# Performance work log

Hardware: AMD Instinct MI355X
Metric: run time of the kernel (lower is better)

## Reference

```python
import jax, jax.numpy as jnp
import numpy as np

B = 2048          # batch
F = 32            # input feature size
H = 512           # lstm hidden size
BN = 64           # autoencoder bottleneck
OUT = 8           # final dense output size
SEQ_LEN = 128
LOOK_AHEAD = 32
RS, RE = 0, 8     # replace_start, replace_end (RE-RS == OUT)


def setup_inputs() -> dict:
    key = jax.random.key(0)
    ks = jax.random.split(key, 16)
    s = lambda k, shape: (jax.random.normal(k, shape, jnp.float32) * 0.05)
    return {
        'x': jax.random.normal(ks[0], (B, SEQ_LEN + LOOK_AHEAD, F), jnp.float32),
        # layer-0 LSTMCell (input F)
        'Wih0': s(ks[1], (F, 4 * H)), 'Whh0': s(ks[2], (H, 4 * H)),
        'bih0': s(ks[3], (4 * H,)),   'bhh0': s(ks[4], (4 * H,)),
        # layer-1 LSTMCell (input H)
        'Wih1': s(ks[5], (H, 4 * H)), 'Whh1': s(ks[6], (H, 4 * H)),
        'bih1': s(ks[7], (4 * H,)),   'bhh1': s(ks[8], (4 * H,)),
        # discretizing autoencoder: 2H -> BN -> 2H (shared across layers)
        'We': s(ks[9], (2 * H, BN)),  'be': s(ks[10], (BN,)),
        'Wd': s(ks[11], (BN, 2 * H)), 'bd': s(ks[12], (2 * H,)),
        # final dense H -> OUT
        'Wf': s(ks[13], (H, OUT)),    'bf': s(ks[14], (OUT,)),
    }


def _lstm_cell(x, h, c, Wih, Whh, bih, bhh):
    # torch.nn.LSTMCell gate order: i, f, g, o
    g = x @ Wih + bih + h @ Whh + bhh          # [B, 4H]
    i, f, gg, o = jnp.split(g, 4, axis=1)
    i, f, o = jax.nn.sigmoid(i), jax.nn.sigmoid(f), jax.nn.sigmoid(o)
    c2 = f * c + i * jnp.tanh(gg)
    return o * jnp.tanh(c2), c2


def _ae(z, We, be, Wd, bd):
    # bottleneck with straight-through rounding (discretization)
    b = jnp.tanh(z @ We + be)
    q = b + jax.lax.stop_gradient(jnp.round(b) - b)
    return q @ Wd + bd


def _layers_fwd(x_t, st, p):
    h0, c0, h1, c1 = st
    hc = _ae(jnp.concatenate([h0, c0], axis=1), p['We'], p['be'], p['Wd'], p['bd'])
    h0, c0 = jnp.split(hc, 2, axis=1)
    h0, c0 = _lstm_cell(x_t, h0, c0, p['Wih0'], p['Whh0'], p['bih0'], p['bhh0'])
    # dropout layer between stacked layers is identity in eval mode
    hc = _ae(jnp.concatenate([h1, c1], axis=1), p['We'], p['be'], p['Wd'], p['bd'])
    h1, c1 = jnp.split(hc, 2, axis=1)
    h1, c1 = _lstm_cell(h0, h1, c1, p['Wih1'], p['Whh1'], p['bih1'], p['bhh1'])
    return (h0, c0, h1, c1)


def reference(x, Wih0, Whh0, bih0, bhh0, Wih1, Whh1, bih1, bhh1,
              We, be, Wd, bd, Wf, bf):
    p = dict(Wih0=Wih0, Whh0=Whh0, bih0=bih0, bhh0=bhh0,
             Wih1=Wih1, Whh1=Whh1, bih1=bih1, bhh1=bhh1,
             We=We, be=be, Wd=Wd, bd=bd)
    bsz = x.shape[0]
    z = jnp.zeros((bsz, H), x.dtype)
    st = (z, z, z, z)

    # warm-up phase over seq_len observed steps
    def step1(st, x_t):
        return _layers_fwd(x_t, st, p), None
    st, _ = jax.lax.scan(step1, st, jnp.swapaxes(x[:, :SEQ_LEN], 0, 1))
    out0 = st[2] @ Wf + bf  # final dense on top-layer h

    def step2(carry, x_t):
        st, out = carry
        x_t = x_t.at[:, RS:RE].set(out)
        st = _layers_fwd(x_t, st, p)
        out = st[2] @ Wf + bf
        return (st, out), out
    (_, _), outs = jax.lax.scan(step2, (st, out0),
                                jnp.swapaxes(x[:, SEQ_LEN:SEQ_LEN + LOOK_AHEAD], 0, 1))

    # [B, 1 + look_ahead, OUT]
    return jnp.concatenate([out0[:, None, :], jnp.swapaxes(outs, 0, 1)], axis=1)
```

## Files before the change

### kernel.cpp

```cpp
#include <hip/hip_runtime.h>
#include <hip/hip_bf16.h>
#include <math.h>

#define NB    2048
#define FIN   32
#define HH    512
#define G4    2048
#define BNE   64
#define OUTD  8
#define SEQL  128
#define LOOK  32
#define TOT   (SEQL + LOOK)
#define TB    8
#define NTHR  1024

__device__ __forceinline__ float sigf(float v) { return 1.0f / (1.0f + expf(-v)); }

#define MAC2(S, HS)                                    \
  {                                                    \
    a[S].x = fmaf(w.x, (HS), a[S].x);                  \
    a[S].y = fmaf(w.y, (HS), a[S].y);                  \
  }
#define MAC2x8()                                       \
  {                                                    \
    MAC2(0, hA.x); MAC2(1, hA.y); MAC2(2, hA.z); MAC2(3, hA.w); \
    MAC2(4, hB.x); MAC2(5, hB.y); MAC2(6, hB.z); MAC2(7, hB.w); \
  }

__global__ __launch_bounds__(NTHR)
void fused_rnn(const float* __restrict__ x,
               const float* __restrict__ Wih0, const float* __restrict__ Whh0,
               const float* __restrict__ bih0, const float* __restrict__ bhh0,
               const float* __restrict__ Wih1, const float* __restrict__ Whh1,
               const float* __restrict__ bih1, const float* __restrict__ bhh1,
               const float* __restrict__ We,   const float* __restrict__ be,
               const float* __restrict__ Wd,   const float* __restrict__ bd,
               const float* __restrict__ Wf,   const float* __restrict__ bf,
               float* __restrict__ out)
{
  __shared__ float sh0[HH][TB], sc0[HH][TB], sh1[HH][TB], sc1[HH][TB];
  __shared__ float sg[TB][G4];
  __shared__ float sq[2][BNE][TB];
  __shared__ float sx[FIN][TB];
  __shared__ float sout[TB][OUTD];

  const int t  = threadIdx.x;
  const int b0 = blockIdx.x * TB;

  for (int i = t; i < HH * TB; i += NTHR) {
    (&sh0[0][0])[i] = 0.f; (&sc0[0][0])[i] = 0.f;
    (&sh1[0][0])[i] = 0.f; (&sc1[0][0])[i] = 0.f;
  }

  const float2 bb0 = make_float2(bih0[2*t]   + bhh0[2*t],
                                 bih0[2*t+1] + bhh0[2*t+1]);
  const float2 bb1 = make_float2(bih1[2*t]   + bhh1[2*t],
                                 bih1[2*t+1] + bhh1[2*t+1]);

  const double Athr = 0.5493061443340549;

  for (int step = 0; step < TOT; ++step) {
    __syncthreads();

    {
      const int ae = t >> 9, s = (t >> 6) & 7, n = t & 63;
      const float* Sh = ae ? &sh1[0][0] : &sh0[0][0];
      const float* Sc = ae ? &sc1[0][0] : &sc0[0][0];
      double a0 = (double)be[n];
      const float* we0 = We + n;
#pragma unroll 4
      for (int k = 0; k < HH; k++)
        a0 = fma((double)Sh[k * TB + s], (double)we0[(size_t)k * BNE], a0);
      const float* we1 = We + (size_t)HH * BNE + n;
#pragma unroll 4
      for (int k = 0; k < HH; k++)
        a0 = fma((double)Sc[k * TB + s], (double)we1[(size_t)k * BNE], a0);
      sq[ae][n][s] = (a0 > Athr) ? 1.f : ((a0 < -Athr) ? -1.f : 0.f);
    }
    __syncthreads();

    {
      float aq0[TB], aq1[TB];
      const float bdv = bd[t];
#pragma unroll
      for (int s = 0; s < TB; s++) { aq0[s] = bdv; aq1[s] = bdv; }
      const float* wd = Wd + t;
#pragma unroll 2
      for (int j = 0; j < BNE; j++) {
        const float w = wd[(size_t)j * (2 * HH)];
        const float4 qA0 = *(const float4*)&sq[0][j][0];
        const float4 qB0 = *(const float4*)&sq[0][j][4];
        const float4 qA1 = *(const float4*)&sq[1][j][0];
        const float4 qB1 = *(const float4*)&sq[1][j][4];
        aq0[0] = fmaf(qA0.x, w, aq0[0]); aq0[1] = fmaf(qA0.y, w, aq0[1]);
        aq0[2] = fmaf(qA0.z, w, aq0[2]); aq0[3] = fmaf(qA0.w, w, aq0[3]);
        aq0[4] = fmaf(qB0.x, w, aq0[4]); aq0[5] = fmaf(qB0.y, w, aq0[5]);
        aq0[6] = fmaf(qB0.z, w, aq0[6]); aq0[7] = fmaf(qB0.w, w, aq0[7]);
        aq1[0] = fmaf(qA1.x, w, aq1[0]); aq1[1] = fmaf(qA1.y, w, aq1[1]);
        aq1[2] = fmaf(qA1.z, w, aq1[2]); aq1[3] = fmaf(qA1.w, w, aq1[3]);
        aq1[4] = fmaf(qB1.x, w, aq1[4]); aq1[5] = fmaf(qB1.y, w, aq1[5]);
        aq1[6] = fmaf(qB1.z, w, aq1[6]); aq1[7] = fmaf(qB1.w, w, aq1[7]);
      }
      if (t < HH) {
#pragma unroll
        for (int s = 0; s < TB; s++) { sh0[t][s] = aq0[s]; sh1[t][s] = aq1[s]; }
      } else {
        const int c = t - HH;
#pragma unroll
        for (int s = 0; s < TB; s++) { sc0[c][s] = aq0[s]; sc1[c][s] = aq1[s]; }
      }
      if (t < FIN * TB) {
        int s = t >> 5, f = t & 31;
        float xv;
        if (step >= SEQL && f < OUTD) xv = sout[s][f];
        else xv = x[((size_t)(b0 + s) * TOT + step) * FIN + f];
        sx[f][s] = xv;
      }
    }
    __syncthreads();

    {
      float2 a[TB];
#pragma unroll
      for (int s = 0; s < TB; s++) a[s] = bb0;
      const float2* wx = (const float2*)Wih0 + t;
#pragma unroll 4
      for (int k = 0; k < FIN; k++) {
        const float2 w  = wx[(size_t)k * (G4 / 2)];
        const float4 hA = *(const float4*)&sx[k][0];
        const float4 hB = *(const float4*)&sx[k][4];
        MAC2x8();
      }
      const float2* wh = (const float2*)Whh0 + t;
#pragma unroll 8
      for (int k = 0; k < HH; k++) {
        const float2 w  = wh[(size_t)k * (G4 / 2)];
        const float4 hA = *(const float4*)&sh0[k][0];
        const float4 hB = *(const float4*)&sh0[k][4];
        MAC2x8();
      }
#pragma unroll
      for (int s = 0; s < TB; s++) *(float2*)&sg[s][2 * t] = a[s];
    }
    __syncthreads();
    {
      const int h  = t & (HH - 1);
      const int sb = (t >> 9) * 4;
#pragma unroll
      for (int s2 = 0; s2 < 4; s2++) {
        const int s = sb + s2;
        const float ig = sigf(sg[s][h]);
        const float fg = sigf(sg[s][HH + h]);
        const float gt = tanhf(sg[s][2 * HH + h]);
        const float og = sigf(sg[s][3 * HH + h]);
        const float c2 = fmaf(fg, sc0[h][s], ig * gt);
        sc0[h][s] = c2;
        sh0[h][s] = og * tanhf(c2);
      }
    }
    __syncthreads();

    {
      float2 a[TB];
#pragma unroll
      for (int s = 0; s < TB; s++) a[s] = bb1;
      const float2* wx = (const float2*)Wih1 + t;
#pragma unroll 8
      for (int k = 0; k < HH; k++) {
        const float2 w  = wx[(size_t)k * (G4 / 2)];
        const float4 hA = *(const float4*)&sh0[k][0];
        const float4 hB = *(const float4*)&sh0[k][4];
        MAC2x8();
      }
      const float2* wh = (const float2*)Whh1 + t;
#pragma unroll 8
      for (int k = 0; k < HH; k++) {
        const float2 w  = wh[(size_t)k * (G4 / 2)];
        const float4 hA = *(const float4*)&sh1[k][0];
        const float4 hB = *(const float4*)&sh1[k][4];
        MAC2x8();
      }
#pragma unroll
      for (int s = 0; s < TB; s++) *(float2*)&sg[s][2 * t] = a[s];
    }
    __syncthreads();
    {
      const int h  = t & (HH - 1);
      const int sb = (t >> 9) * 4;
#pragma unroll
      for (int s2 = 0; s2 < 4; s2++) {
        const int s = sb + s2;
        const float ig = sigf(sg[s][h]);
        const float fg = sigf(sg[s][HH + h]);
        const float gt = tanhf(sg[s][2 * HH + h]);
        const float og = sigf(sg[s][3 * HH + h]);
        const float c2 = fmaf(fg, sc1[h][s], ig * gt);
        sc1[h][s] = c2;
        sh1[h][s] = og * tanhf(c2);
      }
    }

    if (step >= SEQL - 1) {
      __syncthreads();
      if (t < TB * OUTD) {
        int s = t >> 3, o = t & 7;
        float a = bf[o];
#pragma unroll 4
        for (int k = 0; k < HH; k++) a = fmaf(sh1[k][s], Wf[k * OUTD + o], a);
        sout[s][o] = a;
        int slot = step - (SEQL - 1);
        out[((size_t)(b0 + s) * (1 + LOOK) + slot) * OUTD + o] = a;
      }
    }
  }
}

extern "C" void kernel_launch(void* const* d_in, const int* in_sizes, int n_in,
                              void* d_out, int out_size, void* d_ws, size_t ws_size,
                              hipStream_t stream) {
  const float* x    = (const float*)d_in[0];
  const float* Wih0 = (const float*)d_in[1];
  const float* Whh0 = (const float*)d_in[2];
  const float* bih0 = (const float*)d_in[3];
  const float* bhh0 = (const float*)d_in[4];
  const float* Wih1 = (const float*)d_in[5];
  const float* Whh1 = (const float*)d_in[6];
  const float* bih1 = (const float*)d_in[7];
  const float* bhh1 = (const float*)d_in[8];
  const float* We   = (const float*)d_in[9];
  const float* be   = (const float*)d_in[10];
  const float* Wd   = (const float*)d_in[11];
  const float* bd   = (const float*)d_in[12];
  const float* Wf   = (const float*)d_in[13];
  const float* bf   = (const float*)d_in[14];

  fused_rnn<<<NB / TB, NTHR, 0, stream>>>(x, Wih0, Whh0, bih0, bhh0,
                                          Wih1, Whh1, bih1, bhh1,
                                          We, be, Wd, bd, Wf, bf,
                                          (float*)d_out);
}
```

Baseline: 81.12 ms.

## Fuse LSTM gate activation into gate GEMV by remapping threads to hidden units

```diff
diff --git a/kernel.cpp b/kernel.cpp
--- a/kernel.cpp
+++ b/kernel.cpp
@@ -1,5 +1,4 @@
 #include <hip/hip_runtime.h>
-#include <hip/hip_bf16.h>
 #include <math.h>
 
 #define NB    2048
@@ -16,18 +15,11 @@
 
 __device__ __forceinline__ float sigf(float v) { return 1.0f / (1.0f + expf(-v)); }
 
-#define MAC2(S, HS)                                    \
-  {                                                    \
-    a[S].x = fmaf(w.x, (HS), a[S].x);                  \
-    a[S].y = fmaf(w.y, (HS), a[S].y);                  \
-  }
-#define MAC2x8()                                       \
-  {                                                    \
-    MAC2(0, hA.x); MAC2(1, hA.y); MAC2(2, hA.z); MAC2(3, hA.w); \
-    MAC2(4, hB.x); MAC2(5, hB.y); MAC2(6, hB.z); MAC2(7, hB.w); \
-  }
-
-__global__ __launch_bounds__(NTHR)
+#define GMAC2(A, W, HV)                                                  \
+  { A[0].x = fmaf((W).x, (HV).x, A[0].x); A[0].y = fmaf((W).y, (HV).x, A[0].y); \
+    A[1].x = fmaf((W).x, (HV).y, A[1].x); A[1].y = fmaf((W).y, (HV).y, A[1].y); }
+
+__global__ __launch_bounds__(NTHR, 4)
 void fused_rnn(const float* __restrict__ x,
                const float* __restrict__ Wih0, const float* __restrict__ Whh0,
                const float* __restrict__ bih0, const float* __restrict__ bhh0,
@@ -39,8 +31,7 @@
                float* __restrict__ out)
 {
   __shared__ float sh0[HH][TB], sc0[HH][TB], sh1[HH][TB], sc1[HH][TB];
-  __shared__ float sg[TB][G4];
-  __shared__ float sq[2][BNE][TB];
+  __shared__ float tq[2][BNE][TB];
   __shared__ float sx[FIN][TB];
   __shared__ float sout[TB][OUTD];
 
@@ -52,10 +43,21 @@
     (&sh1[0][0])[i] = 0.f; (&sc1[0][0])[i] = 0.f;
   }
 
-  const float2 bb0 = make_float2(bih0[2*t]   + bhh0[2*t],
-                                 bih0[2*t+1] + bhh0[2*t+1]);
-  const float2 bb1 = make_float2(bih1[2*t]   + bhh1[2*t],
-                                 bih1[2*t+1] + bhh1[2*t+1]);
+  const int q   = t & 255;
+  const int sh2 = t >> 8;
+  const int s2  = 2 * sh2;
+  const int u0  = 2 * q;
+  float2 bg0[4], bg1[4];
+#pragma unroll
+  for (int m = 0; m < 4; m++) {
+    const int c = m * HH + u0;
+    bg0[m] = make_float2(bih0[c] + bhh0[c], bih0[c + 1] + bhh0[c + 1]);
+    bg1[m] = make_float2(bih1[c] + bhh1[c], bih1[c + 1] + bhh1[c + 1]);
+  }
+
+  const int ae = t >> 9, sE = (t >> 6) & 7, n = t & 63;
+
+  const float bdc = bd[t];
 
   const double Athr = 0.5493061443340549;
 
@@ -63,51 +65,70 @@
     __syncthreads();
 
     {
-      const int ae = t >> 9, s = (t >> 6) & 7, n = t & 63;
       const float* Sh = ae ? &sh1[0][0] : &sh0[0][0];
       const float* Sc = ae ? &sc1[0][0] : &sc0[0][0];
       double a0 = (double)be[n];
-      const float* we0 = We + n;
+      const float* weh = We + n;
 #pragma unroll 4
       for (int k = 0; k < HH; k++)
-        a0 = fma((double)Sh[k * TB + s], (double)we0[(size_t)k * BNE], a0);
-      const float* we1 = We + (size_t)HH * BNE + n;
+        a0 = fma((double)Sh[k * TB + sE], (double)weh[(size_t)k * BNE], a0);
+      const float* wec = We + (size_t)HH * BNE + n;
 #pragma unroll 4
       for (int k = 0; k < HH; k++)
-        a0 = fma((double)Sc[k * TB + s], (double)we1[(size_t)k * BNE], a0);
-      sq[ae][n][s] = (a0 > Athr) ? 1.f : ((a0 < -Athr) ? -1.f : 0.f);
+        a0 = fma((double)Sc[k * TB + sE], (double)wec[(size_t)k * BNE], a0);
+      tq[ae][n][sE] = (a0 > Athr) ? 1.f : ((a0 < -Athr) ? -1.f : 0.f);
     }
     __syncthreads();
 
     {
-      float aq0[TB], aq1[TB];
-      const float bdv = bd[t];
+      float d0[TB], d1[TB];
 #pragma unroll
-      for (int s = 0; s < TB; s++) { aq0[s] = bdv; aq1[s] = bdv; }
+      for (int s = 0; s < TB; s++) { d0[s] = bdc; d1[s] = bdc; }
       const float* wd = Wd + t;
-#pragma unroll 2
-      for (int j = 0; j < BNE; j++) {
-        const float w = wd[(size_t)j * (2 * HH)];
-        const float4 qA0 = *(const float4*)&sq[0][j][0];
-        const float4 qB0 = *(const float4*)&sq[0][j][4];
-        const float4 qA1 = *(const float4*)&sq[1][j][0];
-        const float4 qB1 = *(const float4*)&sq[1][j][4];
-        aq0[0] = fmaf(qA0.x, w, aq0[0]); aq0[1] = fmaf(qA0.y, w, aq0[1]);
-        aq0[2] = fmaf(qA0.z, w, aq0[2]); aq0[3] = fmaf(qA0.w, w, aq0[3]);
-        aq0[4] = fmaf(qB0.x, w, aq0[4]); aq0[5] = fmaf(qB0.y, w, aq0[5]);
-        aq0[6] = fmaf(qB0.z, w, aq0[6]); aq0[7] = fmaf(qB0.w, w, aq0[7]);
-        aq1[0] = fmaf(qA1.x, w, aq1[0]); aq1[1] = fmaf(qA1.y, w, aq1[1]);
-        aq1[2] = fmaf(qA1.z, w, aq1[2]); aq1[3] = fmaf(qA1.w, w, aq1[3]);
-        aq1[4] = fmaf(qB1.x, w, aq1[4]); aq1[5] = fmaf(qB1.y, w, aq1[5]);
-        aq1[6] = fmaf(qB1.z, w, aq1[6]); aq1[7] = fmaf(qB1.w, w, aq1[7]);
+      float w = wd[0];
+#pragma unroll 4
+      for (int j = 0; j < BNE - 1; j++) {
+        const float wn = wd[(size_t)(j + 1) * (2 * HH)];
+        const float4 qA0 = *(const float4*)&tq[0][j][0];
+        const float4 qB0 = *(const float4*)&tq[0][j][4];
+        const float4 qA1 = *(const float4*)&tq[1][j][0];
+        const float4 qB1 = *(const float4*)&tq[1][j][4];
+        d0[0] = fmaf(qA0.x, w, d0[0]); d0[1] = fmaf(qA0.y, w, d0[1]);
+        d0[2] = fmaf(qA0.z, w, d0[2]); d0[3] = fmaf(qA0.w, w, d0[3]);
+        d0[4] = fmaf(qB0.x, w, d0[4]); d0[5] = fmaf(qB0.y, w, d0[5]);
+        d0[6] = fmaf(qB0.z, w, d0[6]); d0[7] = fmaf(qB0.w, w, d0[7]);
+        d1[0] = fmaf(qA1.x, w, d1[0]); d1[1] = fmaf(qA1.y, w, d1[1]);
+        d1[2] = fmaf(qA1.z, w, d1[2]); d1[3] = fmaf(qA1.w, w, d1[3]);
+        d1[4] = fmaf(qB1.x, w, d1[4]); d1[5] = fmaf(qB1.y, w, d1[5]);
+        d1[6] = fmaf(qB1.z, w, d1[6]); d1[7] = fmaf(qB1.w, w, d1[7]);
+        w = wn;
+      }
+      {
+        const int j = BNE - 1;
+        const float4 qA0 = *(const float4*)&tq[0][j][0];
+        const float4 qB0 = *(const float4*)&tq[0][j][4];
+        const float4 qA1 = *(const float4*)&tq[1][j][0];
+        const float4 qB1 = *(const float4*)&tq[1][j][4];
+        d0[0] = fmaf(qA0.x, w, d0[0]); d0[1] = fmaf(qA0.y, w, d0[1]);
+        d0[2] = fmaf(qA0.z, w, d0[2]); d0[3] = fmaf(qA0.w, w, d0[3]);
+        d0[4] = fmaf(qB0.x, w, d0[4]); d0[5] = fmaf(qB0.y, w, d0[5]);
+        d0[6] = fmaf(qB0.z, w, d0[6]); d0[7] = fmaf(qB0.w, w, d0[7]);
+        d1[0] = fmaf(qA1.x, w, d1[0]); d1[1] = fmaf(qA1.y, w, d1[1]);
+        d1[2] = fmaf(qA1.z, w, d1[2]); d1[3] = fmaf(qA1.w, w, d1[3]);
+        d1[4] = fmaf(qB1.x, w, d1[4]); d1[5] = fmaf(qB1.y, w, d1[5]);
+        d1[6] = fmaf(qB1.z, w, d1[6]); d1[7] = fmaf(qB1.w, w, d1[7]);
       }
       if (t < HH) {
-#pragma unroll
-        for (int s = 0; s < TB; s++) { sh0[t][s] = aq0[s]; sh1[t][s] = aq1[s]; }
+        *(float4*)&sh0[t][0] = make_float4(d0[0], d0[1], d0[2], d0[3]);
+        *(float4*)&sh0[t][4] = make_float4(d0[4], d0[5], d0[6], d0[7]);
+        *(float4*)&sh1[t][0] = make_float4(d1[0], d1[1], d1[2], d1[3]);
+        *(float4*)&sh1[t][4] = make_float4(d1[4], d1[5], d1[6], d1[7]);
       } else {
-        const int c = t - HH;
-#pragma unroll
-        for (int s = 0; s < TB; s++) { sc0[c][s] = aq0[s]; sc1[c][s] = aq1[s]; }
+        const int u = t - HH;
+        *(float4*)&sc0[u][0] = make_float4(d0[0], d0[1], d0[2], d0[3]);
+        *(float4*)&sc0[u][4] = make_float4(d0[4], d0[5], d0[6], d0[7]);
+        *(float4*)&sc1[u][0] = make_float4(d1[0], d1[1], d1[2], d1[3]);
+        *(float4*)&sc1[u][4] = make_float4(d1[4], d1[5], d1[6], d1[7]);
       }
       if (t < FIN * TB) {
         int s = t >> 5, f = t & 31;
@@ -120,84 +141,140 @@
     __syncthreads();
 
     {
-      float2 a[TB];
-#pragma unroll
-      for (int s = 0; s < TB; s++) a[s] = bb0;
-      const float2* wx = (const float2*)Wih0 + t;
-#pragma unroll 4
-      for (int k = 0; k < FIN; k++) {
-        const float2 w  = wx[(size_t)k * (G4 / 2)];
-        const float4 hA = *(const float4*)&sx[k][0];
-        const float4 hB = *(const float4*)&sx[k][4];
-        MAC2x8();
-      }
-      const float2* wh = (const float2*)Whh0 + t;
+      float2 gI[2], gF[2], gG[2], gO[2];
+      gI[0] = gI[1] = bg0[0]; gF[0] = gF[1] = bg0[1];
+      gG[0] = gG[1] = bg0[2]; gO[0] = gO[1] = bg0[3];
+      {
+        const float* row = Wih0 + u0;
+#pragma unroll 4
+        for (int k = 0; k < FIN; k++, row += G4) {
+          const float2 wI = *(const float2*)(row);
+          const float2 wF = *(const float2*)(row + HH);
+          const float2 wG = *(const float2*)(row + 2 * HH);
+          const float2 wO = *(const float2*)(row + 3 * HH);
+          const float2 hv = *(const float2*)&sx[k][s2];
+          GMAC2(gI, wI, hv); GMAC2(gF, wF, hv); GMAC2(gG, wG, hv); GMAC2(gO, wO, hv);
+        }
+      }
+      {
+        const float* row = Whh0 + u0;
+        float2 wI = *(const float2*)(row);
+        float2 wF = *(const float2*)(row + HH);
+        float2 wG = *(const float2*)(row + 2 * HH);
+        float2 wO = *(const float2*)(row + 3 * HH);
+        row += G4;
 #pragma unroll 8
-      for (int k = 0; k < HH; k++) {
-        const float2 w  = wh[(size_t)k * (G4 / 2)];
-        const float4 hA = *(const float4*)&sh0[k][0];
-        const float4 hB = *(const float4*)&sh0[k][4];
-        MAC2x8();
-      }
-#pragma unroll
-      for (int s = 0; s < TB; s++) *(float2*)&sg[s][2 * t] = a[s];
+        for (int k = 0; k < HH - 1; k++, row += G4) {
+          const float2 nI = *(const float2*)(row);
+          const float2 nF = *(const float2*)(row + HH);
+          const float2 nG = *(const float2*)(row + 2 * HH);
+          const float2 nO = *(const float2*)(row + 3 * HH);
+          const float2 hv = *(const float2*)&sh0[k][s2];
+          GMAC2(gI, wI, hv); GMAC2(gF, wF, hv); GMAC2(gG, wG, hv); GMAC2(gO, wO, hv);
+          wI = nI; wF = nF; wG = nG; wO = nO;
+        }
+        const float2 hv = *(const float2*)&sh0[HH - 1][s2];
+        GMAC2(gI, wI, hv); GMAC2(gF, wF, hv); GMAC2(gG, wG, hv); GMAC2(gO, wO, hv);
+      }
+      const float2 cA = *(const float2*)&sc0[u0][s2];
+      const float2 cB = *(const float2*)&sc0[u0 + 1][s2];
+      float2 hA2, hB2, cA2, cB2;
+      {
+        float ig = sigf(gI[0].x), fg = sigf(gF[0].x);
+        float gt = tanhf(gG[0].x), og = sigf(gO[0].x);
+        float c2 = fmaf(fg, cA.x, ig * gt);
+        cA2.x = c2; hA2.x = og * tanhf(c2);
+        ig = sigf(gI[0].y); fg = sigf(gF[0].y);
+        gt = tanhf(gG[0].y); og = sigf(gO[0].y);
+        c2 = fmaf(fg, cB.x, ig * gt);
+        cB2.x = c2; hB2.x = og * tanhf(c2);
+        ig = sigf(gI[1].x); fg = sigf(gF[1].x);
+        gt = tanhf(gG[1].x); og = sigf(gO[1].x);
+        c2 = fmaf(fg, cA.y, ig * gt);
+        cA2.y = c2; hA2.y = og * tanhf(c2);
+        ig = sigf(gI[1].y); fg = sigf(gF[1].y);
+        gt = tanhf(gG[1].y); og = sigf(gO[1].y);
+        c2 = fmaf(fg, cB.y, ig * gt);
+        cB2.y = c2; hB2.y = og * tanhf(c2);
+      }
+      __syncthreads();
+      *(float2*)&sh0[u0][s2]     = hA2;
+      *(float2*)&sh0[u0 + 1][s2] = hB2;
+      *(float2*)&sc0[u0][s2]     = cA2;
+      *(float2*)&sc0[u0 + 1][s2] = cB2;
     }
     __syncthreads();
+
     {
-      const int h  = t & (HH - 1);
-      const int sb = (t >> 9) * 4;
-#pragma unroll
-      for (int s2 = 0; s2 < 4; s2++) {
-        const int s = sb + s2;
-        const float ig = sigf(sg[s][h]);
-        const float fg = sigf(sg[s][HH + h]);
-        const float gt = tanhf(sg[s][2 * HH + h]);
-        const float og = sigf(sg[s][3 * HH + h]);
-        const float c2 = fmaf(fg, sc0[h][s], ig * gt);
-        sc0[h][s] = c2;
-        sh0[h][s] = og * tanhf(c2);
-      }
-    }
-    __syncthreads();
-
-    {
-      float2 a[TB];
-#pragma unroll
-      for (int s = 0; s < TB; s++) a[s] = bb1;
-      const float2* wx = (const float2*)Wih1 + t;
+      float2 gI[2], gF[2], gG[2], gO[2];
+      gI[0] = gI[1] = bg1[0]; gF[0] = gF[1] = bg1[1];
+      gG[0] = gG[1] = bg1[2]; gO[0] = gO[1] = bg1[3];
+      {
+        const float* row = Wih1 + u0;
+        float2 wI = *(const float2*)(row);
+        float2 wF = *(const float2*)(row + HH);
+        float2 wG = *(const float2*)(row + 2 * HH);
+        float2 wO = *(const float2*)(row + 3 * HH);
+        row += G4;
 #pragma unroll 8
-      for (int k = 0; k < HH; k++) {
-        const float2 w  = wx[(size_t)k * (G4 / 2)];
-        const float4 hA = *(const float4*)&sh0[k][0];
-        const float4 hB = *(const float4*)&sh0[k][4];
-        MAC2x8();
-      }
-      const float2* wh = (const float2*)Whh1 + t;
+        for (int k = 0; k < HH - 1; k++, row += G4) {
+          const float2 nI = *(const float2*)(row);
+          const float2 nF = *(const float2*)(row + HH);
+          const float2 nG = *(const float2*)(row + 2 * HH);
+          const float2 nO = *(const float2*)(row + 3 * HH);
+          const float2 hv = *(const float2*)&sh0[k][s2];
+          GMAC2(gI, wI, hv); GMAC2(gF, wF, hv); GMAC2(gG, wG, hv); GMAC2(gO, wO, hv);
+          wI = nI; wF = nF; wG = nG; wO = nO;
+        }
+        const float2 hv = *(const float2*)&sh0[HH - 1][s2];
+        GMAC2(gI, wI, hv); GMAC2(gF, wF, hv); GMAC2(gG, wG, hv); GMAC2(gO, wO, hv);
+      }
+      {
+        const float* row = Whh1 + u0;
+        float2 wI = *(const float2*)(row);
+        float2 wF = *(const float2*)(row + HH);
+        float2 wG = *(const float2*)(row + 2 * HH);
+        float2 wO = *(const float2*)(row + 3 * HH);
+        row += G4;
 #pragma unroll 8
-      for (int k = 0; k < HH; k++) {
-        const float2 w  = wh[(size_t)k * (G4 / 2)];
-        const float4 hA = *(const float4*)&sh1[k][0];
-        const float4 hB = *(const float4*)&sh1[k][4];
-        MAC2x8();
-      }
-#pragma unroll
-      for (int s = 0; s < TB; s++) *(float2*)&sg[s][2 * t] = a[s];
-    }
-    __syncthreads();
-    {
-      const int h  = t & (HH - 1);
-      const int sb = (t >> 9) * 4;
-#pragma unroll
-      for (int s2 = 0; s2 < 4; s2++) {
-        const int s = sb + s2;
-        const float ig = sigf(sg[s][h]);
-        const float fg = sigf(sg[s][HH + h]);
-        const float gt = tanhf(sg[s][2 * HH + h]);
-        const float og = sigf(sg[s][3 * HH + h]);
-        const float c2 = fmaf(fg, sc1[h][s], ig * gt);
-        sc1[h][s] = c2;
-        sh1[h][s] = og * tanhf(c2);
-      }
+        for (int k = 0; k < HH - 1; k++, row += G4) {
+          const float2 nI = *(const float2*)(row);
+          const float2 nF = *(const float2*)(row + HH);
+          const float2 nG = *(const float2*)(row + 2 * HH);
+          const float2 nO = *(const float2*)(row + 3 * HH);
+          const float2 hv = *(const float2*)&sh1[k][s2];
+          GMAC2(gI, wI, hv); GMAC2(gF, wF, hv); GMAC2(gG, wG, hv); GMAC2(gO, wO, hv);
+          wI = nI; wF = nF; wG = nG; wO = nO;
+        }
+        const float2 hv = *(const float2*)&sh1[HH - 1][s2];
+        GMAC2(gI, wI, hv); GMAC2(gF, wF, hv); GMAC2(gG, wG, hv); GMAC2(gO, wO, hv);
+      }
+      const float2 cA = *(const float2*)&sc1[u0][s2];
+      const float2 cB = *(const float2*)&sc1[u0 + 1][s2];
+      float2 hA2, hB2, cA2, cB2;
+      {
+        float ig = sigf(gI[0].x), fg = sigf(gF[0].x);
+        float gt = tanhf(gG[0].x), og = sigf(gO[0].x);
+        float c2 = fmaf(fg, cA.x, ig * gt);
+        cA2.x = c2; hA2.x = og * tanhf(c2);
+        ig = sigf(gI[0].y); fg = sigf(gF[0].y);
+        gt = tanhf(gG[0].y); og = sigf(gO[0].y);
+        c2 = fmaf(fg, cB.x, ig * gt);
+        cB2.x = c2; hB2.x = og * tanhf(c2);
+        ig = sigf(gI[1].x); fg = sigf(gF[1].x);
+        gt = tanhf(gG[1].x); og = sigf(gO[1].x);
+        c2 = fmaf(fg, cA.y, ig * gt);
+        cA2.y = c2; hA2.y = og * tanhf(c2);
+        ig = sigf(gI[1].y); fg = sigf(gF[1].y);
+        gt = tanhf(gG[1].y); og = sigf(gO[1].y);
+        c2 = fmaf(fg, cB.y, ig * gt);
+        cB2.y = c2; hB2.y = og * tanhf(c2);
+      }
+      __syncthreads();
+      *(float2*)&sh1[u0][s2]     = hA2;
+      *(float2*)&sh1[u0 + 1][s2] = hB2;
+      *(float2*)&sc1[u0][s2]     = cA2;
+      *(float2*)&sc1[u0 + 1][s2] = cB2;
     }
 
     if (step >= SEQL - 1) {
```

After: 127.7 ms. 57.5% more time.

## Double-buffer LSTM weight chunks through LDS with register prefetch

Applied to the files above, without the earlier changes.

```diff
diff --git a/kernel.cpp b/kernel.cpp
--- a/kernel.cpp
+++ b/kernel.cpp
@@ -1,5 +1,4 @@
 #include <hip/hip_runtime.h>
-#include <hip/hip_bf16.h>
 #include <math.h>
 
 #define NB    2048
@@ -13,6 +12,7 @@
 #define TOT   (SEQL + LOOK)
 #define TB    8
 #define NTHR  1024
+#define BK    4
 
 __device__ __forceinline__ float sigf(float v) { return 1.0f / (1.0f + expf(-v)); }
 
@@ -25,6 +25,26 @@
   {                                                    \
     MAC2(0, hA.x); MAC2(1, hA.y); MAC2(2, hA.z); MAC2(3, hA.w); \
     MAC2(4, hB.x); MAC2(5, hB.y); MAC2(6, hB.z); MAC2(7, hB.w); \
+  }
+
+#define STAGE_ISSUE(W, CH)                                              \
+  { const float4* gp = (const float4*)((W) + (size_t)(CH) * BK * G4);   \
+    r0 = gp[t]; r1 = gp[t + NTHR]; }
+#define STAGE_WRITE(B)                                                  \
+  { ((float4*)&smem[(B) * (BK * G4)])[t] = r0;                          \
+    ((float4*)&smem[(B) * (BK * G4)])[t + NTHR] = r1; }
+
+#define CHUNK_COMPUTE(SROW)                                             \
+  {                                                                     \
+    const float* wb = &smem[cur * (BK * G4)];                           \
+    _Pragma("unroll")                                                   \
+    for (int kk = 0; kk < BK; kk++) {                                   \
+      const float2 w  = *(const float2*)&wb[kk * G4 + 2 * t];           \
+      const float*  sr = (SROW);                                        \
+      const float4 hA = *(const float4*)&sr[0];                         \
+      const float4 hB = *(const float4*)&sr[4];                         \
+      MAC2x8();                                                         \
+    }                                                                   \
   }
 
 __global__ __launch_bounds__(NTHR)
@@ -39,10 +59,12 @@
                float* __restrict__ out)
 {
   __shared__ float sh0[HH][TB], sc0[HH][TB], sh1[HH][TB], sc1[HH][TB];
-  __shared__ float sg[TB][G4];
+  __shared__ float smem[2 * BK * G4];
   __shared__ float sq[2][BNE][TB];
   __shared__ float sx[FIN][TB];
   __shared__ float sout[TB][OUTD];
+
+#define SG(S, C) smem[(S) * G4 + (C)]
 
   const int t  = threadIdx.x;
   const int b0 = blockIdx.x * TB;
@@ -123,24 +145,29 @@
       float2 a[TB];
 #pragma unroll
       for (int s = 0; s < TB; s++) a[s] = bb0;
-      const float2* wx = (const float2*)Wih0 + t;
-#pragma unroll 4
-      for (int k = 0; k < FIN; k++) {
-        const float2 w  = wx[(size_t)k * (G4 / 2)];
-        const float4 hA = *(const float4*)&sx[k][0];
-        const float4 hB = *(const float4*)&sx[k][4];
-        MAC2x8();
-      }
-      const float2* wh = (const float2*)Whh0 + t;
-#pragma unroll 8
-      for (int k = 0; k < HH; k++) {
-        const float2 w  = wh[(size_t)k * (G4 / 2)];
-        const float4 hA = *(const float4*)&sh0[k][0];
-        const float4 hB = *(const float4*)&sh0[k][4];
-        MAC2x8();
-      }
-#pragma unroll
-      for (int s = 0; s < TB; s++) *(float2*)&sg[s][2 * t] = a[s];
+      float4 r0, r1;
+      int cur = 0;
+      STAGE_ISSUE(Wih0, 0);
+      STAGE_WRITE(0);
+      __syncthreads();
+      for (int c = 0; c < FIN / BK; c++) {
+        if (c < FIN / BK - 1) STAGE_ISSUE(Wih0, c + 1)
+        else                  STAGE_ISSUE(Whh0, 0);
+        CHUNK_COMPUTE(&sx[BK * c + kk][0]);
+        STAGE_WRITE(cur ^ 1);
+        __syncthreads();
+        cur ^= 1;
+      }
+      for (int c = 0; c < HH / BK; c++) {
+        const bool pf = (c < HH / BK - 1);
+        if (pf) STAGE_ISSUE(Whh0, c + 1);
+        CHUNK_COMPUTE(&sh0[BK * c + kk][0]);
+        if (pf) STAGE_WRITE(cur ^ 1);
+        __syncthreads();
+        cur ^= 1;
+      }
+#pragma unroll
+      for (int s = 0; s < TB; s++) *(float2*)&SG(s, 2 * t) = a[s];
     }
     __syncthreads();
     {
@@ -149,10 +176,10 @@
 #pragma unroll
       for (int s2 = 0; s2 < 4; s2++) {
         const int s = sb + s2;
-        const float ig = sigf(sg[s][h]);
-        const float fg = sigf(sg[s][HH + h]);
-        const float gt = tanhf(sg[s][2 * HH + h]);
-        const float og = sigf(sg[s][3 * HH + h]);
+        const float ig = sigf(SG(s, h));
+        const float fg = sigf(SG(s, HH + h));
+        const float gt = tanhf(SG(s, 2 * HH + h));
+        const float og = sigf(SG(s, 3 * HH + h));
         const float c2 = fmaf(fg, sc0[h][s], ig * gt);
         sc0[h][s] = c2;
         sh0[h][s] = og * tanhf(c2);
@@ -164,24 +191,29 @@
       float2 a[TB];
 #pragma unroll
       for (int s = 0; s < TB; s++) a[s] = bb1;
-      const float2* wx = (const float2*)Wih1 + t;
-#pragma unroll 8
-      for (int k = 0; k < HH; k++) {
-        const float2 w  = wx[(size_t)k * (G4 / 2)];
-        const float4 hA = *(const float4*)&sh0[k][0];
-        const float4 hB = *(const float4*)&sh0[k][4];
-        MAC2x8();
-      }
-      const float2* wh = (const float2*)Whh1 + t;
-#pragma unroll 8
-      for (int k = 0; k < HH; k++) {
-        const float2 w  = wh[(size_t)k * (G4 / 2)];
-        const float4 hA = *(const float4*)&sh1[k][0];
-        const float4 hB = *(const float4*)&sh1[k][4];
-        MAC2x8();
-      }
-#pragma unroll
-      for (int s = 0; s < TB; s++) *(float2*)&sg[s][2 * t] = a[s];
+      float4 r0, r1;
+      int cur = 0;
+      STAGE_ISSUE(Wih1, 0);
+      STAGE_WRITE(0);
+      __syncthreads();
+      for (int c = 0; c < HH / BK; c++) {
+        if (c < HH / BK - 1) STAGE_ISSUE(Wih1, c + 1)
+        else                 STAGE_ISSUE(Whh1, 0);
+        CHUNK_COMPUTE(&sh0[BK * c + kk][0]);
+        STAGE_WRITE(cur ^ 1);
+        __syncthreads();
+        cur ^= 1;
+      }
+      for (int c = 0; c < HH / BK; c++) {
+        const bool pf = (c < HH / BK - 1);
+        if (pf) STAGE_ISSUE(Whh1, c + 1);
+        CHUNK_COMPUTE(&sh1[BK * c + kk][0]);
+        if (pf) STAGE_WRITE(cur ^ 1);
+        __syncthreads();
+        cur ^= 1;
+      }
+#pragma unroll
+      for (int s = 0; s < TB; s++) *(float2*)&SG(s, 2 * t) = a[s];
     }
     __syncthreads();
     {
@@ -190,10 +222,10 @@
 #pragma unroll
       for (int s2 = 0; s2 < 4; s2++) {
         const int s = sb + s2;
-        const float ig = sigf(sg[s][h]);
-        const float fg = sigf(sg[s][HH + h]);
-        const float gt = tanhf(sg[s][2 * HH + h]);
-        const float og = sigf(sg[s][3 * HH + h]);
+        const float ig = sigf(SG(s, h));
+        const float fg = sigf(SG(s, HH + h));
+        const float gt = tanhf(SG(s, 2 * HH + h));
+        const float og = sigf(SG(s, 3 * HH + h));
         const float c2 = fmaf(fg, sc1[h][s], ig * gt);
         sc1[h][s] = c2;
         sh1[h][s] = og * tanhf(c2);
@@ -213,6 +245,7 @@
       }
     }
   }
+#undef SG
 }
 
 extern "C" void kernel_launch(void* const* d_in, const int* in_sizes, int n_in,
```

Result: slower. 92.56 ms (+14.1%).

## Retile LSTM gate matvecs to 4 gates x 4 batch per thread with pipelined float4 loads

Applied to the files above, without the earlier changes.

```diff
diff --git a/kernel.cpp b/kernel.cpp
--- a/kernel.cpp
+++ b/kernel.cpp
@@ -1,5 +1,4 @@
 #include <hip/hip_runtime.h>
-#include <hip/hip_bf16.h>
 #include <math.h>
 
 #define NB    2048
@@ -16,18 +15,52 @@
 
 __device__ __forceinline__ float sigf(float v) { return 1.0f / (1.0f + expf(-v)); }
 
-#define MAC2(S, HS)                                    \
-  {                                                    \
-    a[S].x = fmaf(w.x, (HS), a[S].x);                  \
-    a[S].y = fmaf(w.y, (HS), a[S].y);                  \
-  }
-#define MAC2x8()                                       \
-  {                                                    \
-    MAC2(0, hA.x); MAC2(1, hA.y); MAC2(2, hA.z); MAC2(3, hA.w); \
-    MAC2(4, hB.x); MAC2(5, hB.y); MAC2(6, hB.z); MAC2(7, hB.w); \
-  }
-
-__global__ __launch_bounds__(NTHR)
+#define FMA4x4(W, HV)                                   \
+  { acc[0].x = fmaf((W).x, (HV).x, acc[0].x);           \
+    acc[0].y = fmaf((W).y, (HV).x, acc[0].y);           \
+    acc[0].z = fmaf((W).z, (HV).x, acc[0].z);           \
+    acc[0].w = fmaf((W).w, (HV).x, acc[0].w);           \
+    acc[1].x = fmaf((W).x, (HV).y, acc[1].x);           \
+    acc[1].y = fmaf((W).y, (HV).y, acc[1].y);           \
+    acc[1].z = fmaf((W).z, (HV).y, acc[1].z);           \
+    acc[1].w = fmaf((W).w, (HV).y, acc[1].w);           \
+    acc[2].x = fmaf((W).x, (HV).z, acc[2].x);           \
+    acc[2].y = fmaf((W).y, (HV).z, acc[2].y);           \
+    acc[2].z = fmaf((W).z, (HV).z, acc[2].z);           \
+    acc[2].w = fmaf((W).w, (HV).z, acc[2].w);           \
+    acc[3].x = fmaf((W).x, (HV).w, acc[3].x);           \
+    acc[3].y = fmaf((W).y, (HV).w, acc[3].y);           \
+    acc[3].z = fmaf((W).z, (HV).w, acc[3].z);           \
+    acc[3].w = fmaf((W).w, (HV).w, acc[3].w); }
+
+#define LOADBLK(DST, WP, KB)                            \
+  { _Pragma("unroll")                                   \
+    for (int i = 0; i < 8; i++)                         \
+      DST[i] = (WP)[((KB) * 8 + i) * (G4 / 4)]; }
+
+#define FMABLK(SRC, KB, STATE)                          \
+  { _Pragma("unroll")                                   \
+    for (int i = 0; i < 8; i++) {                       \
+      const float4 hv = *(const float4*)&STATE[(KB) * 8 + i][4 * v]; \
+      FMA4x4(SRC[i], hv);                               \
+    } }
+
+#define K512_PIPE(WPTR, STATE)                          \
+  { const float4* wp = (const float4*)(WPTR) + q;       \
+    float4 wa[8], wb[8];                                \
+    LOADBLK(wa, wp, 0)                                  \
+    _Pragma("unroll 1")                                 \
+    for (int kb = 0; kb < 31; kb++) {                   \
+      LOADBLK(wb, wp, 2 * kb + 1)                       \
+      FMABLK(wa, 2 * kb, STATE)                         \
+      LOADBLK(wa, wp, 2 * kb + 2)                       \
+      FMABLK(wb, 2 * kb + 1, STATE)                     \
+    }                                                   \
+    LOADBLK(wb, wp, 63)                                 \
+    FMABLK(wa, 62, STATE)                               \
+    FMABLK(wb, 63, STATE) }
+
+__global__ __launch_bounds__(NTHR, 4)
 void fused_rnn(const float* __restrict__ x,
                const float* __restrict__ Wih0, const float* __restrict__ Whh0,
                const float* __restrict__ bih0, const float* __restrict__ bhh0,
@@ -52,10 +85,14 @@
     (&sh1[0][0])[i] = 0.f; (&sc1[0][0])[i] = 0.f;
   }
 
-  const float2 bb0 = make_float2(bih0[2*t]   + bhh0[2*t],
-                                 bih0[2*t+1] + bhh0[2*t+1]);
-  const float2 bb1 = make_float2(bih1[2*t]   + bhh1[2*t],
-                                 bih1[2*t+1] + bhh1[2*t+1]);
+  const int q = t & 511, v = t >> 9;
+  float4 bg0, bg1;
+  { const float4 a = *(const float4*)&bih0[4 * q];
+    const float4 b = *(const float4*)&bhh0[4 * q];
+    bg0 = make_float4(a.x + b.x, a.y + b.y, a.z + b.z, a.w + b.w); }
+  { const float4 a = *(const float4*)&bih1[4 * q];
+    const float4 b = *(const float4*)&bhh1[4 * q];
+    bg1 = make_float4(a.x + b.x, a.y + b.y, a.z + b.z, a.w + b.w); }
 
   const double Athr = 0.5493061443340549;
 
@@ -120,27 +157,23 @@
     __syncthreads();
 
     {
-      float2 a[TB];
-#pragma unroll
-      for (int s = 0; s < TB; s++) a[s] = bb0;
-      const float2* wx = (const float2*)Wih0 + t;
-#pragma unroll 4
-      for (int k = 0; k < FIN; k++) {
-        const float2 w  = wx[(size_t)k * (G4 / 2)];
-        const float4 hA = *(const float4*)&sx[k][0];
-        const float4 hB = *(const float4*)&sx[k][4];
-        MAC2x8();
-      }
-      const float2* wh = (const float2*)Whh0 + t;
-#pragma unroll 8
-      for (int k = 0; k < HH; k++) {
-        const float2 w  = wh[(size_t)k * (G4 / 2)];
-        const float4 hA = *(const float4*)&sh0[k][0];
-        const float4 hB = *(const float4*)&sh0[k][4];
-        MAC2x8();
-      }
-#pragma unroll
-      for (int s = 0; s < TB; s++) *(float2*)&sg[s][2 * t] = a[s];
+      float4 acc[4];
+      acc[0] = bg0; acc[1] = bg0; acc[2] = bg0; acc[3] = bg0;
+      {
+        const float4* wp = (const float4*)Wih0 + q;
+        float4 wa[8], wb[8];
+        LOADBLK(wa, wp, 0)
+        LOADBLK(wb, wp, 1)
+        FMABLK(wa, 0, sx)
+        LOADBLK(wa, wp, 2)
+        FMABLK(wb, 1, sx)
+        LOADBLK(wb, wp, 3)
+        FMABLK(wa, 2, sx)
+        FMABLK(wb, 3, sx)
+      }
+      K512_PIPE(Whh0, sh0)
+#pragma unroll
+      for (int s = 0; s < 4; s++) *(float4*)&sg[4 * v + s][4 * q] = acc[s];
     }
     __syncthreads();
     {
@@ -161,27 +194,12 @@
     __syncthreads();
 
     {
-      float2 a[TB];
-#pragma unroll
-      for (int s = 0; s < TB; s++) a[s] = bb1;
-      const float2* wx = (const float2*)Wih1 + t;
-#pragma unroll 8
-      for (int k = 0; k < HH; k++) {
-        const float2 w  = wx[(size_t)k * (G4 / 2)];
-        const float4 hA = *(const float4*)&sh0[k][0];
-        const float4 hB = *(const float4*)&sh0[k][4];
-        MAC2x8();
-      }
-      const float2* wh = (const float2*)Whh1 + t;
-#pragma unroll 8
-      for (int k = 0; k < HH; k++) {
-        const float2 w  = wh[(size_t)k * (G4 / 2)];
-        const float4 hA = *(const float4*)&sh1[k][0];
-        const float4 hB = *(const float4*)&sh1[k][4];
-        MAC2x8();
-      }
-#pragma unroll
-      for (int s = 0; s < TB; s++) *(float2*)&sg[s][2 * t] = a[s];
+      float4 acc[4];
+      acc[0] = bg1; acc[1] = bg1; acc[2] = bg1; acc[3] = bg1;
+      K512_PIPE(Wih1, sh0)
+      K512_PIPE(Whh1, sh1)
+#pragma unroll
+      for (int s = 0; s < 4; s++) *(float4*)&sg[4 * v + s][4 * q] = acc[s];
     }
     __syncthreads();
     {
```

New measurement: 113.4 ms. +39.8%, slower.
